# Performance work log

Hardware: AMD Instinct MI355X
Metric: run time of the kernel (lower is better)

Reference implementation:

```python
import jax, jax.numpy as jnp
import numpy as np
from jax.scipy.special import logsumexp

B, T, K, D = 512, 500, 64, 64  # n_batch, timesteps, n_latent_kcs (=n_chains), latent_dim


def setup_inputs() -> dict:
    key = jax.random.key(0)
    k1, k2, k3, k4, k5 = jax.random.split(key, 5)
    corr = jax.random.randint(k1, (B, T), 0, 2)                      # binary observations
    kc_idx = jax.random.randint(k2, (B, T), 0, K)
    chain = jax.nn.one_hot(kc_idx, K, dtype=jnp.float32)             # hard gumbel sample, [B,T,K]
    kc_embd_weight = jax.random.normal(k3, (K, D), dtype=jnp.float32)
    kc_f_weight = jax.random.normal(k4, (5, D), dtype=jnp.float32) * (1.0 / np.sqrt(D))
    kc_f_bias = jax.random.normal(k5, (5,), dtype=jnp.float32) * 0.01
    return {"corr": corr, "chain": chain, "kc_embd_weight": kc_embd_weight,
            "kc_f_weight": kc_f_weight, "kc_f_bias": kc_f_bias}


def _bkt_forward(corr, chain, kc_embd_weight, kc_f_weight, kc_f_bias):
    # kc_logits_f(kc_embd.weight): [K,5]
    l = kc_embd_weight @ kc_f_weight.T + kc_f_bias
    # hstack((-l0,l1,l0,-l1)).reshape(-1,2,2) -> trans[k] = [[-l0,l1],[l0,-l1]] (Target,Source)
    trans_logits = jnp.stack([-l[:, 0], l[:, 1], l[:, 0], -l[:, 1]], axis=1).reshape(K, 2, 2)
    obs_logits = jnp.stack([-l[:, 2], l[:, 2], l[:, 3], -l[:, 3]], axis=1).reshape(K, 2, 2)
    init_logits = jnp.stack([-l[:, 4], l[:, 4]], axis=1)             # [K,2]

    log_obs = jax.nn.log_softmax(obs_logits, axis=2)                 # [K,states,outputs]
    log_t = jax.nn.log_softmax(trans_logits, axis=1)                 # [K,target,source]
    log_alpha0 = jnp.broadcast_to(jax.nn.log_softmax(init_logits, axis=1), (B, K, 2))

    def step(log_alpha, xs):
        c, y = xs                                                    # c:[B,K] one-hot, y:[B]
        # emission prediction: a1[b,s,o] = sum_k c[b,k] * log_obs[k,s,o]
        a1 = jnp.einsum('bk,kso->bso', c, log_obs)                   # [B,2,2]
        a2 = jnp.einsum('bk,bks->bs', c, log_alpha)                  # [B,2]
        lp = logsumexp(a1 + a2[:, :, None], axis=1)                  # [B,2]
        log_py = lp - logsumexp(lp, axis=1, keepdims=True)
        # filtering update with observed y
        lp_y = jnp.take_along_axis(a1, y[:, None, None], axis=2)[:, :, 0]   # [B,2] = log p(y_b | s)
        a2t = jnp.einsum('bk,kts->bts', c, log_t)                    # [B,target,source]
        a3 = logsumexp(lp_y[:, None, :] + a2[:, None, :] + a2t, axis=2)     # [B,2]
        new_alpha = (1.0 - c)[:, :, None] * log_alpha + c[:, :, None] * a3[:, None, :]
        return new_alpha, log_py

    xs = (jnp.transpose(chain, (1, 0, 2)), corr.T)                   # time-major for scan
    _, outs = jax.lax.scan(step, log_alpha0, xs)                     # outs: [T,B,2]
    return jnp.transpose(outs, (1, 0, 2))                            # [B,T,2]


def reference(corr, chain, kc_embd_weight, kc_f_weight, kc_f_bias):
    return _bkt_forward(corr, chain, kc_embd_weight, kc_f_weight, kc_f_bias)
```

## Files before the change

### kernel.cpp

```cpp
#include <hip/hip_runtime.h>
#include <stdint.h>

#define BB 512
#define TT 500
#define KK 64
#define DD 64
#define WPB 4

typedef unsigned long long ull;


__launch_bounds__(256, 4)
__global__ void ev_stream(const uint32_t* __restrict__ chainw,
                          const int* __restrict__ corr,
                          const float* __restrict__ embd,
                          const float* __restrict__ Wf,
                          const float* __restrict__ bias,
                          ull* __restrict__ tbm,
                          ull* __restrict__ ybm,
                          float4* __restrict__ params4,
                          float* __restrict__ p1i) {
    if (blockIdx.x == 0 && threadIdx.x < KK) {
        const int k = threadIdx.x;
        float l0 = bias[0], l1 = bias[1], l2 = bias[2], l3 = bias[3], l4 = bias[4];
        const float4* er = (const float4*)(embd + k * DD);
        const float4* w0 = (const float4*)(Wf + 0 * DD);
        const float4* w1 = (const float4*)(Wf + 1 * DD);
        const float4* w2 = (const float4*)(Wf + 2 * DD);
        const float4* w3 = (const float4*)(Wf + 3 * DD);
        const float4* w4 = (const float4*)(Wf + 4 * DD);
#pragma unroll 4
        for (int d4 = 0; d4 < DD / 4; ++d4) {
            float4 e = er[d4];
            float4 a;
            a = w0[d4]; l0 = fmaf(e.x,a.x,fmaf(e.y,a.y,fmaf(e.z,a.z,fmaf(e.w,a.w,l0))));
            a = w1[d4]; l1 = fmaf(e.x,a.x,fmaf(e.y,a.y,fmaf(e.z,a.z,fmaf(e.w,a.w,l1))));
            a = w2[d4]; l2 = fmaf(e.x,a.x,fmaf(e.y,a.y,fmaf(e.z,a.z,fmaf(e.w,a.w,l2))));
            a = w3[d4]; l3 = fmaf(e.x,a.x,fmaf(e.y,a.y,fmaf(e.z,a.z,fmaf(e.w,a.w,l3))));
            a = w4[d4]; l4 = fmaf(e.x,a.x,fmaf(e.y,a.y,fmaf(e.z,a.z,fmaf(e.w,a.w,l4))));
        }
        auto sig = [](float x) { return 1.0f / (1.0f + __expf(-x)); };
        params4[k] = make_float4(sig(2.f*l2),
                                 sig(-2.f*l3),
                                 sig(2.f*l0),
                                 sig(-2.f*l1));
        p1i[k] = sig(2.f*l4);
    }

    const int lane = threadIdx.x & 63;
    const int wv = threadIdx.x >> 6;
    uint32_t sv = chainw[lane];
    ull sm = __ballot(sv != 0u);
    const bool isb = (__popcll(sm) >= 2);

    const int wid = blockIdx.x * WPB + wv;
    const int b = wid >> 3, w = wid & 7;
    const int t = w * 64 + lane;
    const bool live = (t < TT);

    __shared__ ull tmask[WPB][KK];
    __shared__ ull ymask[WPB][KK];
    tmask[wv][lane] = 0;
    ymask[wv][lane] = 0;

    int y = 0;
    if (live) y = corr[b * TT + t] & 1;

    int k = -1;
    if (isb) {
        const uint4* rp = (const uint4*)chainw + (((size_t)b * TT + t) << 3);
        if (live) {
            uint4 r[8];
#pragma unroll
            for (int q = 0; q < 8; ++q) r[q] = rp[q];
#pragma unroll
            for (int q = 0; q < 8; ++q) {
                uint4 v = r[q];
                if ((v.x | v.y | v.z | v.w) != 0u) {
                    int widx; uint32_t nw;
                    if (v.x)      { widx = 0; nw = v.x; }
                    else if (v.y) { widx = 1; nw = v.y; }
                    else if (v.z) { widx = 2; nw = v.z; }
                    else          { widx = 3; nw = v.w; }
                    k = q * 8 + widx * 2 + ((nw >> 16) ? 1 : 0);
                }
            }
        }
    } else {
        const uint4* rp = (const uint4*)chainw + (((size_t)b * TT + t) << 4);
        if (live) {
            uint4 r[16];
#pragma unroll
            for (int q = 0; q < 16; ++q) r[q] = rp[q];
#pragma unroll
            for (int q = 0; q < 16; ++q) {
                uint4 v = r[q];
                if ((v.x | v.y | v.z | v.w) != 0u) {
                    int widx;
                    if (v.x)      widx = 0;
                    else if (v.y) widx = 1;
                    else if (v.z) widx = 2;
                    else          widx = 3;
                    k = q * 4 + widx;
                }
            }
        }
    }

    if (k >= 0) {
        atomicOr(&tmask[wv][k], 1ull << lane);
        if (y) atomicOr(&ymask[wv][k], 1ull << lane);
    }

    const size_t o = (((size_t)b * 8 + w) << 6) + lane;
    tbm[o] = tmask[wv][lane];
    ybm[o] = ymask[wv][lane];
}

__launch_bounds__(128, 8)
__global__ void bkt_bits(const ull* __restrict__ tbm,
                         const ull* __restrict__ ybm,
                         const float4* __restrict__ params4,
                         const float* __restrict__ p1i,
                         float2* __restrict__ out) {
    const int lane = threadIdx.x & 63;
    const int b = blockIdx.x * 2 + (threadIdx.x >> 6);

    const ull* tp = tbm + ((size_t)b << 9) + lane;
    const ull* yp = ybm + ((size_t)b << 9) + lane;
    ull tm[8], ym[8];
#pragma unroll
    for (int w = 0; w < 8; ++w) tm[w] = tp[(size_t)w << 6];
#pragma unroll
    for (int w = 0; w < 8; ++w) ym[w] = yp[(size_t)w << 6];

    const float4 P = params4[lane];
    const float g0 = P.x, g1 = P.y, t10 = P.z, t11 = P.w;
    const float dg = g1 - g0, dt = t11 - t10, g1c = 1.f - g1;
    float p1 = p1i[lane];

    float2* ob = out + (size_t)b * TT;
#pragma unroll
    for (int w = 0; w < 8; ++w) {
        ull tb = tm[w];
        const ull yb = ym[w];
        while (tb) {
            int j = __builtin_ctzll(tb);
            tb &= tb - 1;
            int t = w * 64 + j;
            int y = (int)((yb >> j) & 1ull);
            float pe1 = fmaf(p1, dg, g0);
            float pe0 = 1.f - pe1;
            ob[t] = make_float2(__logf(pe0), __logf(pe1));
            float gy  = y ? g1  : g1c;
            float pyy = y ? pe1 : pe0;
            p1 = fmaf(p1 * __fdividef(gy, pyy), dt, t10);
        }
    }
}

extern "C" void kernel_launch(void* const* d_in, const int* in_sizes, int n_in,
                              void* d_out, int out_size, void* d_ws, size_t ws_size,
                              hipStream_t stream) {
    const void* p_corr = nullptr, *p_chain = nullptr, *p_embd = nullptr,
              * p_Wf = nullptr, *p_bias = nullptr;
    for (int i = 0; i < n_in; ++i) {
        switch (in_sizes[i]) {
            case BB * TT:        p_corr  = d_in[i]; break;
            case BB * TT * KK:   p_chain = d_in[i]; break;
            case KK * DD:        p_embd  = d_in[i]; break;
            case 5 * DD:         p_Wf    = d_in[i]; break;
            case 5:              p_bias  = d_in[i]; break;
            default: break;
        }
    }
    if (!p_corr)  p_corr  = d_in[0];
    if (!p_chain) p_chain = d_in[1];
    if (!p_embd)  p_embd  = d_in[2];
    if (!p_Wf)    p_Wf    = d_in[3];
    if (!p_bias)  p_bias  = d_in[4];
    (void)out_size;

    const size_t PLANE = (size_t)BB * 8 * KK * 8;
    ull*    tbm     = (ull*)d_ws;
    ull*    ybm     = (ull*)((char*)d_ws + PLANE);
    float4* params4 = (float4*)((char*)d_ws + 2 * PLANE);
    float*  p1i     = (float*)((char*)d_ws + 2 * PLANE + KK * 16);

    ev_stream<<<BB * 8 / WPB, 64 * WPB, 0, stream>>>(
        (const uint32_t*)p_chain, (const int*)p_corr,
        (const float*)p_embd, (const float*)p_Wf, (const float*)p_bias,
        tbm, ybm, params4, p1i);
    bkt_bits<<<BB / 2, 128, 0, stream>>>(tbm, ybm, params4, p1i, (float2*)d_out);
}
```

Measured before the change: 25.66 us.

## Fuse bitmask build and BKT recurrence into one per-batch kernel

Merges the two kernels into one, with one 512-thread block per batch row. The block builds the per-chain time bitmasks in shared memory and then runs the sequential recurrence from shared memory, so the global workspace round trip and the second launch go away. Each block now recomputes the small parameter projection for its wave 0, which repeats a little work per block. Only one wave does the serial scan while seven waves sit idle, and the scan can no longer overlap with streaming of the chain tensor across launches.

```diff
diff --git a/kernel.cpp b/kernel.cpp
--- a/kernel.cpp
+++ b/kernel.cpp
@@ -5,63 +5,32 @@
 #define TT 500
 #define KK 64
 #define DD 64
-#define WPB 4
 
 typedef unsigned long long ull;
 
-
-__launch_bounds__(256, 4)
-__global__ void ev_stream(const uint32_t* __restrict__ chainw,
+__launch_bounds__(512, 4)
+__global__ void bkt_fused(const uint32_t* __restrict__ chainw,
                           const int* __restrict__ corr,
                           const float* __restrict__ embd,
                           const float* __restrict__ Wf,
                           const float* __restrict__ bias,
-                          ull* __restrict__ tbm,
-                          ull* __restrict__ ybm,
-                          float4* __restrict__ params4,
-                          float* __restrict__ p1i) {
-    if (blockIdx.x == 0 && threadIdx.x < KK) {
-        const int k = threadIdx.x;
-        float l0 = bias[0], l1 = bias[1], l2 = bias[2], l3 = bias[3], l4 = bias[4];
-        const float4* er = (const float4*)(embd + k * DD);
-        const float4* w0 = (const float4*)(Wf + 0 * DD);
-        const float4* w1 = (const float4*)(Wf + 1 * DD);
-        const float4* w2 = (const float4*)(Wf + 2 * DD);
-        const float4* w3 = (const float4*)(Wf + 3 * DD);
-        const float4* w4 = (const float4*)(Wf + 4 * DD);
-#pragma unroll 4
-        for (int d4 = 0; d4 < DD / 4; ++d4) {
-            float4 e = er[d4];
-            float4 a;
-            a = w0[d4]; l0 = fmaf(e.x,a.x,fmaf(e.y,a.y,fmaf(e.z,a.z,fmaf(e.w,a.w,l0))));
-            a = w1[d4]; l1 = fmaf(e.x,a.x,fmaf(e.y,a.y,fmaf(e.z,a.z,fmaf(e.w,a.w,l1))));
-            a = w2[d4]; l2 = fmaf(e.x,a.x,fmaf(e.y,a.y,fmaf(e.z,a.z,fmaf(e.w,a.w,l2))));
-            a = w3[d4]; l3 = fmaf(e.x,a.x,fmaf(e.y,a.y,fmaf(e.z,a.z,fmaf(e.w,a.w,l3))));
-            a = w4[d4]; l4 = fmaf(e.x,a.x,fmaf(e.y,a.y,fmaf(e.z,a.z,fmaf(e.w,a.w,l4))));
-        }
-        auto sig = [](float x) { return 1.0f / (1.0f + __expf(-x)); };
-        params4[k] = make_float4(sig(2.f*l2),
-                                 sig(-2.f*l3),
-                                 sig(2.f*l0),
-                                 sig(-2.f*l1));
-        p1i[k] = sig(2.f*l4);
-    }
+                          float2* __restrict__ out) {
+    __shared__ ull tmask[8][KK];
+    __shared__ ull ymask[8][KK];
 
-    const int lane = threadIdx.x & 63;
-    const int wv = threadIdx.x >> 6;
+    const int b = blockIdx.x;
+    const int tid = threadIdx.x;
+    const int wv = tid >> 6, lane = tid & 63;
+
     uint32_t sv = chainw[lane];
     ull sm = __ballot(sv != 0u);
     const bool isb = (__popcll(sm) >= 2);
 
-    const int wid = blockIdx.x * WPB + wv;
-    const int b = wid >> 3, w = wid & 7;
-    const int t = w * 64 + lane;
-    const bool live = (t < TT);
-
-    __shared__ ull tmask[WPB][KK];
-    __shared__ ull ymask[WPB][KK];
     tmask[wv][lane] = 0;
     ymask[wv][lane] = 0;
+
+    const int t = wv * 64 + lane;
+    const bool live = (t < TT);
 
     int y = 0;
     if (live) y = corr[b * TT + t] & 1;
@@ -107,54 +76,58 @@
         }
     }
 
+    float g0, g1, t10, t11, p1;
+    if (wv == 0) {
+        float l0 = bias[0], l1 = bias[1], l2 = bias[2], l3 = bias[3], l4 = bias[4];
+        const float4* er = (const float4*)(embd + lane * DD);
+        const float4* w0 = (const float4*)(Wf + 0 * DD);
+        const float4* w1 = (const float4*)(Wf + 1 * DD);
+        const float4* w2 = (const float4*)(Wf + 2 * DD);
+        const float4* w3 = (const float4*)(Wf + 3 * DD);
+        const float4* w4 = (const float4*)(Wf + 4 * DD);
+#pragma unroll 4
+        for (int d4 = 0; d4 < DD / 4; ++d4) {
+            float4 e = er[d4];
+            float4 a;
+            a = w0[d4]; l0 = fmaf(e.x,a.x,fmaf(e.y,a.y,fmaf(e.z,a.z,fmaf(e.w,a.w,l0))));
+            a = w1[d4]; l1 = fmaf(e.x,a.x,fmaf(e.y,a.y,fmaf(e.z,a.z,fmaf(e.w,a.w,l1))));
+            a = w2[d4]; l2 = fmaf(e.x,a.x,fmaf(e.y,a.y,fmaf(e.z,a.z,fmaf(e.w,a.w,l2))));
+            a = w3[d4]; l3 = fmaf(e.x,a.x,fmaf(e.y,a.y,fmaf(e.z,a.z,fmaf(e.w,a.w,l3))));
+            a = w4[d4]; l4 = fmaf(e.x,a.x,fmaf(e.y,a.y,fmaf(e.z,a.z,fmaf(e.w,a.w,l4))));
+        }
+        auto sig = [](float x) { return 1.0f / (1.0f + __expf(-x)); };
+        t10 = sig( 2.f * l0);
+        t11 = sig(-2.f * l1);
+        g0  = sig( 2.f * l2);
+        g1  = sig(-2.f * l3);
+        p1  = sig( 2.f * l4);
+    }
+
     if (k >= 0) {
         atomicOr(&tmask[wv][k], 1ull << lane);
         if (y) atomicOr(&ymask[wv][k], 1ull << lane);
     }
+    __syncthreads();
 
-    const size_t o = (((size_t)b * 8 + w) << 6) + lane;
-    tbm[o] = tmask[wv][lane];
-    ybm[o] = ymask[wv][lane];
-}
-
-__launch_bounds__(128, 8)
-__global__ void bkt_bits(const ull* __restrict__ tbm,
-                         const ull* __restrict__ ybm,
-                         const float4* __restrict__ params4,
-                         const float* __restrict__ p1i,
-                         float2* __restrict__ out) {
-    const int lane = threadIdx.x & 63;
-    const int b = blockIdx.x * 2 + (threadIdx.x >> 6);
-
-    const ull* tp = tbm + ((size_t)b << 9) + lane;
-    const ull* yp = ybm + ((size_t)b << 9) + lane;
-    ull tm[8], ym[8];
+    if (wv == 0) {
+        const float dg = g1 - g0, dt = t11 - t10, g1c = 1.f - g1;
+        float2* ob = out + (size_t)b * TT;
 #pragma unroll
-    for (int w = 0; w < 8; ++w) tm[w] = tp[(size_t)w << 6];
-#pragma unroll
-    for (int w = 0; w < 8; ++w) ym[w] = yp[(size_t)w << 6];
-
-    const float4 P = params4[lane];
-    const float g0 = P.x, g1 = P.y, t10 = P.z, t11 = P.w;
-    const float dg = g1 - g0, dt = t11 - t10, g1c = 1.f - g1;
-    float p1 = p1i[lane];
-
-    float2* ob = out + (size_t)b * TT;
-#pragma unroll
-    for (int w = 0; w < 8; ++w) {
-        ull tb = tm[w];
-        const ull yb = ym[w];
-        while (tb) {
-            int j = __builtin_ctzll(tb);
-            tb &= tb - 1;
-            int t = w * 64 + j;
-            int y = (int)((yb >> j) & 1ull);
-            float pe1 = fmaf(p1, dg, g0);
-            float pe0 = 1.f - pe1;
-            ob[t] = make_float2(__logf(pe0), __logf(pe1));
-            float gy  = y ? g1  : g1c;
-            float pyy = y ? pe1 : pe0;
-            p1 = fmaf(p1 * __fdividef(gy, pyy), dt, t10);
+        for (int w = 0; w < 8; ++w) {
+            ull tb = tmask[w][lane];
+            const ull yb = ymask[w][lane];
+            while (tb) {
+                int j = __builtin_ctzll(tb);
+                tb &= tb - 1;
+                int tt = w * 64 + j;
+                int yy = (int)((yb >> j) & 1ull);
+                float pe1 = fmaf(p1, dg, g0);
+                float pe0 = 1.f - pe1;
+                ob[tt] = make_float2(__logf(pe0), __logf(pe1));
+                float gy  = yy ? g1  : g1c;
+                float pyy = yy ? pe1 : pe0;
+                p1 = fmaf(p1 * __fdividef(gy, pyy), dt, t10);
+            }
         }
     }
 }
@@ -179,17 +152,12 @@
     if (!p_embd)  p_embd  = d_in[2];
     if (!p_Wf)    p_Wf    = d_in[3];
     if (!p_bias)  p_bias  = d_in[4];
-    (void)out_size;
+    (void)d_ws; (void)ws_size; (void)out_size;
 
-    const size_t PLANE = (size_t)BB * 8 * KK * 8;
-    ull*    tbm     = (ull*)d_ws;
-    ull*    ybm     = (ull*)((char*)d_ws + PLANE);
-    float4* params4 = (float4*)((char*)d_ws + 2 * PLANE);
-    float*  p1i     = (float*)((char*)d_ws + 2 * PLANE + KK * 16);
-
-    ev_stream<<<BB * 8 / WPB, 64 * WPB, 0, stream>>>(
-        (const uint32_t*)p_chain, (const int*)p_corr,
-        (const float*)p_embd, (const float*)p_Wf, (const float*)p_bias,
-        tbm, ybm, params4, p1i);
-    bkt_bits<<<BB / 2, 128, 0, stream>>>(tbm, ybm, params4, p1i, (float2*)d_out);
+    bkt_fused<<<BB, 512, 0, stream>>>((const uint32_t*)p_chain,
+                                      (const int*)p_corr,
+                                      (const float*)p_embd,
+                                      (const float*)p_Wf,
+                                      (const float*)p_bias,
+                                      (float2*)d_out);
 }
```

Result: faster. 22.52 us, median of 2 (-12.2%).
